# Optimization experiments

Measured on AMD Instinct MI355X. Metric: run time of the kernel, lower is better.

Reference implementation:

```python
import jax, jax.numpy as jnp
import numpy as np

B, S, H, D = 16, 2048, 768, 128
ATTR_MAX, ITEMS_MAX = 8, 32  # static equivalents of attr_type_ids.max() / item_position_ids max (data generated to hit these)


def setup_inputs() -> dict:
    key = jax.random.key(0)
    k1, k2, k3, k4 = jax.random.split(key, 4)
    return {
        "attention_mask": jnp.ones((B, S), dtype=jnp.int32),
        "hidden_states": jax.random.normal(k1, (B, S, H), dtype=jnp.float32),
        "attr_type_ids": jax.random.randint(k2, (B, S), 0, ATTR_MAX + 1),
        "item_position_ids": jax.random.randint(k3, (B, S), 0, ITEMS_MAX + 1),
        "W": jax.random.normal(k4, (H, D), dtype=jnp.float32) * (1.0 / np.sqrt(H)),
        "b": jnp.zeros((D,), dtype=jnp.float32),
    }


def reference(attention_mask, hidden_states, attr_type_ids, item_position_ids, W, b):
    # linear projection: [B,S,H] @ [H,D] -> [B,S,D]
    h = jnp.einsum('bsh,hd->bsd', hidden_states, W) + b
    Bn, Sn, Dn = h.shape

    # segmented mean over (attr_id, item_id) groups; attr/item id 0 (and >max, e.g. the 50 pad sentinel) are invalid
    valid = (attr_type_ids >= 1) & (attr_type_ids <= ATTR_MAX) & \
            (item_position_ids >= 1) & (item_position_ids <= ITEMS_MAX)
    batch_idx = jnp.arange(Bn)[:, None]
    seg = (batch_idx * ATTR_MAX + (attr_type_ids - 1)) * ITEMS_MAX + (item_position_ids - 1)
    nseg = Bn * ATTR_MAX * ITEMS_MAX
    seg = jnp.where(valid, seg, nseg)  # dump invalid tokens into extra segment
    flat_seg = seg.reshape(-1)

    sums = jax.ops.segment_sum(h.reshape(-1, Dn), flat_seg, num_segments=nseg + 1)[:nseg]
    counts = jax.ops.segment_sum(valid.reshape(-1).astype(h.dtype), flat_seg, num_segments=nseg + 1)[:nseg]

    sums = sums.reshape(Bn, ATTR_MAX, ITEMS_MAX, Dn)
    counts = counts.reshape(Bn, ATTR_MAX, ITEMS_MAX)
    empty = counts == 0
    pooled = sums / jnp.where(empty, jnp.ones_like(counts), counts)[..., None]
    return pooled, empty, h
```

## Files before the change

kernel.cpp:

```cpp
#include <hip/hip_runtime.h>
#include <hip/hip_bf16.h>

#define Bn 16
#define Sn 2048
#define Hn 768
#define Dn 128
#define AT 8
#define IT 32
#define NSEG (Bn*AT*IT)

typedef __attribute__((ext_vector_type(4))) float f32x4;
typedef __attribute__((ext_vector_type(2))) float f32x2;
typedef __attribute__((ext_vector_type(4))) int   i32x4;
typedef __attribute__((ext_vector_type(8))) short bf16x8;
typedef __attribute__((ext_vector_type(4))) short s16x4;

__device__ __forceinline__ unsigned short f2bf(float f){
  union { float f; unsigned u; } v; v.f = f;
  unsigned r = v.u + 0x7FFFu + ((v.u >> 16) & 1u);
  return (unsigned short)(r >> 16);
}

__global__ __launch_bounds__(256) void k_prep(const float* __restrict__ W,
                                              unsigned short* __restrict__ Wt){
  int gid = blockIdx.x*256 + threadIdx.x;
  if (gid >= Hn*Dn) return;
  int d = gid / Hn;
  int k = gid - d*Hn;
  Wt[gid] = f2bf(W[k*Dn + d]);
}

__global__ __launch_bounds__(256) void k_gemm(const float* __restrict__ X,
        const unsigned short* __restrict__ Wt, const float* __restrict__ bias,
        float* __restrict__ Hout){
  __shared__ unsigned char sA[2][64*128];
  __shared__ unsigned char sB[2][128*128];
  const int tid  = threadIdx.x;
  const int lane = tid & 63;
  const int wave = tid >> 6;
  const int m0 = blockIdx.x * 64;

  const int ar = tid >> 2, akq = tid & 3;
  const int bc = tid >> 1, bkh = tid & 1;
  const float*          Ap = X  + (size_t)(m0 + ar)*Hn + akq*4;
  const unsigned short* Bp = Wt + (size_t)bc*Hn + bkh*32;

  int aw[4], bw[4];
  #pragma unroll
  for (int c=0;c<4;c++) aw[c] = ar*128 + ((akq*8 + c*32) ^ ((ar&7)<<4));
  #pragma unroll
  for (int c=0;c<4;c++) bw[c] = bc*128 + ((bkh*64 + c*16) ^ ((bc&7)<<4));

  int abase[4], aswz[4];
  #pragma unroll
  for (int mi=0;mi<4;mi++){
    int row = mi*16 + (lane&15);
    abase[mi] = row*128; aswz[mi] = (row&7)<<4;
  }
  int bbase[2], bswz[2];
  #pragma unroll
  for (int ni=0;ni<2;ni++){
    int col = wave*32 + ni*16 + (lane&15);
    bbase[ni] = col*128; bswz[ni] = (col&7)<<4;
  }
  const int kblk = (lane>>4)*16;

  f32x4 acc[4][2];
  #pragma unroll
  for (int mi=0;mi<4;mi++)
    #pragma unroll
    for (int ni=0;ni<2;ni++) acc[mi][ni] = (f32x4){0.f,0.f,0.f,0.f};

  f32x4 av[4]; i32x4 bv[4];
  #pragma unroll
  for (int c=0;c<4;c++) av[c] = *(const f32x4*)(Ap + c*16);
  #pragma unroll
  for (int c=0;c<4;c++) bv[c] = *(const i32x4*)(Bp + c*8);
  #pragma unroll
  for (int c=0;c<4;c++){
    s16x4 t;
    t[0]=(short)f2bf(av[c][0]); t[1]=(short)f2bf(av[c][1]);
    t[2]=(short)f2bf(av[c][2]); t[3]=(short)f2bf(av[c][3]);
    *(s16x4*)&sA[0][aw[c]] = t;
  }
  #pragma unroll
  for (int c=0;c<4;c++) *(i32x4*)&sB[0][bw[c]] = bv[c];
  __syncthreads();

  int cur = 0;
  for (int step=0; step<12; ++step){
    if (step < 11){
      #pragma unroll
      for (int c=0;c<4;c++) av[c] = *(const f32x4*)(Ap + (step+1)*64 + c*16);
      #pragma unroll
      for (int c=0;c<4;c++) bv[c] = *(const i32x4*)(Bp + (step+1)*64 + c*8);
    }
    #pragma unroll
    for (int ks=0; ks<2; ++ks){
      bf16x8 af[4], bfv[2];
      #pragma unroll
      for (int mi=0;mi<4;mi++)
        af[mi] = *(const bf16x8*)&sA[cur][abase[mi] + ((ks*64 + kblk) ^ aswz[mi])];
      #pragma unroll
      for (int ni=0;ni<2;ni++)
        bfv[ni] = *(const bf16x8*)&sB[cur][bbase[ni] + ((ks*64 + kblk) ^ bswz[ni])];
      #pragma unroll
      for (int mi=0;mi<4;mi++)
        #pragma unroll
        for (int ni=0;ni<2;ni++)
          acc[mi][ni] = __builtin_amdgcn_mfma_f32_16x16x32_bf16(af[mi], bfv[ni], acc[mi][ni], 0, 0, 0);
    }
    if (step < 11){
      #pragma unroll
      for (int c=0;c<4;c++){
        s16x4 t;
        t[0]=(short)f2bf(av[c][0]); t[1]=(short)f2bf(av[c][1]);
        t[2]=(short)f2bf(av[c][2]); t[3]=(short)f2bf(av[c][3]);
        *(s16x4*)&sA[cur^1][aw[c]] = t;
      }
      #pragma unroll
      for (int c=0;c<4;c++) *(i32x4*)&sB[cur^1][bw[c]] = bv[c];
    }
    __syncthreads();
    cur ^= 1;
  }

  #pragma unroll
  for (int ni=0;ni<2;ni++){
    int col = wave*32 + ni*16 + (lane&15);
    float bb = bias[col];
    #pragma unroll
    for (int mi=0;mi<4;mi++){
      int row0 = m0 + mi*16 + (lane>>4)*4;
      #pragma unroll
      for (int r=0;r<4;r++)
        Hout[(size_t)(row0 + r)*Dn + col] = acc[mi][ni][r] + bb;
    }
  }
}

__global__ __launch_bounds__(256) void k_scan(const int* __restrict__ attr,
        const int* __restrict__ item, const float* __restrict__ Hsrc,
        float* __restrict__ pooled, float* __restrict__ empty){
  __shared__ float ssum[4][IT][Dn];
  __shared__ int   slist[4][512];
  __shared__ int   scnt[IT];

  const int wg  = blockIdx.x;
  const int a   = wg & 7;
  const int b   = wg >> 3;
  const int tid = threadIdx.x;
  const int wv  = tid >> 6;
  const int lane = tid & 63;

  for (int i = tid; i < 4*IT*Dn; i += 256) (&ssum[0][0][0])[i] = 0.f;
  if (tid < IT) scnt[tid] = 0;
  __syncthreads();

  const int tok0 = wv * 512;
  const int gbase = b * Sn;
  int nm = 0;
  #pragma unroll
  for (int g = 0; g < 8; ++g){
    int tok = tok0 + g*64 + lane;
    int avv = attr[gbase + tok], ivv = item[gbase + tok];
    bool m = (avv == a+1) && (ivv >= 1) && (ivv <= IT);
    unsigned long long mask = __ballot(m);
    int pos = nm + __popcll(mask & ((1ull << lane) - 1ull));
    if (m){
      slist[wv][pos] = ((ivv-1) << 16) | tok;
      atomicAdd(&scnt[ivv-1], 1);
    }
    nm += __popcll(mask);
  }

  const f32x2* hb = (const f32x2*)(Hsrc + (size_t)b*Sn*Dn);
  float* myacc = &ssum[wv][0][0];
  int e = 0;
  for (; e + 8 <= nm; e += 8){
    int idx[8]; f32x2 v[8];
    #pragma unroll
    for (int j=0;j<8;j++) idx[j] = slist[wv][e+j];
    #pragma unroll
    for (int j=0;j<8;j++) v[j] = hb[(size_t)(idx[j] & 0xffff)*64 + lane];
    #pragma unroll
    for (int j=0;j<8;j++){
      f32x2* p = (f32x2*)&myacc[(idx[j]>>16)*Dn + lane*2];
      f32x2 old = *p; old[0] += v[j][0]; old[1] += v[j][1]; *p = old;
    }
  }
  for (; e < nm; ++e){
    int idx = slist[wv][e];
    f32x2 v = hb[(size_t)(idx & 0xffff)*64 + lane];
    f32x2* p = (f32x2*)&myacc[(idx>>16)*Dn + lane*2];
    f32x2 old = *p; old[0] += v[0]; old[1] += v[1]; *p = old;
  }
  __syncthreads();

  float* outp = pooled + (size_t)wg*IT*Dn;
  for (int o = tid; o < IT*Dn; o += 256){
    int i = o >> 7, d = o & 127;
    float s = ssum[0][i][d] + ssum[1][i][d] + ssum[2][i][d] + ssum[3][i][d];
    int cnt = scnt[i];
    outp[o] = s / (float)(cnt > 0 ? cnt : 1);
  }
  if (tid < IT) empty[wg*IT + tid] = (scnt[tid] == 0) ? 1.f : 0.f;
}

extern "C" void kernel_launch(void* const* d_in, const int* in_sizes, int n_in,
                              void* d_out, int out_size, void* d_ws, size_t ws_size,
                              hipStream_t stream) {
  const float* hidden = (const float*)d_in[1];
  const int*   attr   = (const int*)  d_in[2];
  const int*   item   = (const int*)  d_in[3];
  const float* W      = (const float*)d_in[4];
  const float* bias   = (const float*)d_in[5];

  float* pooled = (float*)d_out;
  float* empty  = pooled + (size_t)NSEG*Dn;
  float* Hout   = empty  + NSEG;

  unsigned short* Wt = (unsigned short*)d_ws;

  k_prep<<<(Hn*Dn + 255)/256, 256, 0, stream>>>(W, Wt);
  k_gemm<<<(Bn*Sn)/64, 256, 0, stream>>>(hidden, Wt, bias, Hout);
  k_scan<<<Bn*AT, 256, 0, stream>>>(attr, item, Hout, pooled, empty);
}
```

Baseline: 42.27 us.

## Tile W transpose through shared memory and split segment scan across D halves

The weight prep kernel now transposes W in 64x64 tiles through padded shared memory, so global reads and writes are coalesced and the bf16 stores are vectorised. The scan kernel splits each (batch, attr) block into two blocks that each own half of the D dimension. This doubles the grid to 256 workgroups and halves the shared-memory accumulator. Count atomics move after the list build, spread across lanes. The cost is that each half-block re-reads the attr/item ids, and gathers become scalar float loads instead of float2.

```diff
diff --git a/kernel.cpp b/kernel.cpp
--- a/kernel.cpp
+++ b/kernel.cpp
@@ -10,7 +10,6 @@
 #define NSEG (Bn*AT*IT)
 
 typedef __attribute__((ext_vector_type(4))) float f32x4;
-typedef __attribute__((ext_vector_type(2))) float f32x2;
 typedef __attribute__((ext_vector_type(4))) int   i32x4;
 typedef __attribute__((ext_vector_type(8))) short bf16x8;
 typedef __attribute__((ext_vector_type(4))) short s16x4;
@@ -23,11 +22,29 @@
 
 __global__ __launch_bounds__(256) void k_prep(const float* __restrict__ W,
                                               unsigned short* __restrict__ Wt){
-  int gid = blockIdx.x*256 + threadIdx.x;
-  if (gid >= Hn*Dn) return;
-  int d = gid / Hn;
-  int k = gid - d*Hn;
-  Wt[gid] = f2bf(W[k*Dn + d]);
+  __shared__ float sT[64][65];
+  const int tid = threadIdx.x;
+  const int k0 = (blockIdx.x % 12) * 64;
+  const int d0 = (blockIdx.x / 12) * 64;
+  const int rr = tid >> 4;
+  const int cg = tid & 15;
+
+  #pragma unroll
+  for (int p = 0; p < 4; ++p){
+    int k = rr + p*16;
+    f32x4 v = *(const f32x4*)&W[(size_t)(k0 + k)*Dn + d0 + cg*4];
+    sT[k][cg*4+0] = v[0]; sT[k][cg*4+1] = v[1];
+    sT[k][cg*4+2] = v[2]; sT[k][cg*4+3] = v[3];
+  }
+  __syncthreads();
+  #pragma unroll
+  for (int p = 0; p < 4; ++p){
+    int d = rr + p*16;
+    s16x4 t;
+    #pragma unroll
+    for (int j = 0; j < 4; ++j) t[j] = (short)f2bf(sT[cg*4+j][d]);
+    *(s16x4*)&Wt[(size_t)(d0 + d)*Hn + k0 + cg*4] = t;
+  }
 }
 
 __global__ __launch_bounds__(256) void k_gemm(const float* __restrict__ X,
@@ -142,20 +159,21 @@
 __global__ __launch_bounds__(256) void k_scan(const int* __restrict__ attr,
         const int* __restrict__ item, const float* __restrict__ Hsrc,
         float* __restrict__ pooled, float* __restrict__ empty){
-  __shared__ float ssum[4][IT][Dn];
+  __shared__ float ssum[4][IT][64];
   __shared__ int   slist[4][512];
   __shared__ int   scnt[IT];
 
   const int wg  = blockIdx.x;
-  const int a   = wg & 7;
-  const int b   = wg >> 3;
+  const int dh  = wg & 1;
+  const int a   = (wg >> 1) & 7;
+  const int b   = wg >> 4;
   const int tid = threadIdx.x;
   const int wv  = tid >> 6;
   const int lane = tid & 63;
 
-  for (int i = tid; i < 4*IT*Dn; i += 256) (&ssum[0][0][0])[i] = 0.f;
+  #pragma unroll
+  for (int i = 0; i < IT; ++i) ssum[wv][i][lane] = 0.f;
   if (tid < IT) scnt[tid] = 0;
-  __syncthreads();
 
   const int tok0 = wv * 512;
   const int gbase = b * Sn;
@@ -167,44 +185,39 @@
     bool m = (avv == a+1) && (ivv >= 1) && (ivv <= IT);
     unsigned long long mask = __ballot(m);
     int pos = nm + __popcll(mask & ((1ull << lane) - 1ull));
-    if (m){
-      slist[wv][pos] = ((ivv-1) << 16) | tok;
-      atomicAdd(&scnt[ivv-1], 1);
-    }
+    if (m) slist[wv][pos] = ((ivv-1) << 16) | tok;
     nm += __popcll(mask);
   }
-
-  const f32x2* hb = (const f32x2*)(Hsrc + (size_t)b*Sn*Dn);
-  float* myacc = &ssum[wv][0][0];
+  __syncthreads();
+
+  for (int e = lane; e < nm; e += 64) atomicAdd(&scnt[slist[wv][e] >> 16], 1);
+
+  const float* hb = Hsrc + (size_t)b*Sn*Dn + dh*64 + lane;
   int e = 0;
   for (; e + 8 <= nm; e += 8){
-    int idx[8]; f32x2 v[8];
+    int idx[8]; float v[8];
     #pragma unroll
     for (int j=0;j<8;j++) idx[j] = slist[wv][e+j];
     #pragma unroll
-    for (int j=0;j<8;j++) v[j] = hb[(size_t)(idx[j] & 0xffff)*64 + lane];
-    #pragma unroll
-    for (int j=0;j<8;j++){
-      f32x2* p = (f32x2*)&myacc[(idx[j]>>16)*Dn + lane*2];
-      f32x2 old = *p; old[0] += v[j][0]; old[1] += v[j][1]; *p = old;
-    }
+    for (int j=0;j<8;j++) v[j] = hb[(size_t)(idx[j] & 0xffff)*Dn];
+    #pragma unroll
+    for (int j=0;j<8;j++) ssum[wv][idx[j]>>16][lane] += v[j];
   }
   for (; e < nm; ++e){
     int idx = slist[wv][e];
-    f32x2 v = hb[(size_t)(idx & 0xffff)*64 + lane];
-    f32x2* p = (f32x2*)&myacc[(idx>>16)*Dn + lane*2];
-    f32x2 old = *p; old[0] += v[0]; old[1] += v[1]; *p = old;
-  }
-  __syncthreads();
-
-  float* outp = pooled + (size_t)wg*IT*Dn;
-  for (int o = tid; o < IT*Dn; o += 256){
-    int i = o >> 7, d = o & 127;
+    ssum[wv][idx>>16][lane] += hb[(size_t)(idx & 0xffff)*Dn];
+  }
+  __syncthreads();
+
+  float* outp = pooled + (size_t)(b*AT + a)*IT*Dn + dh*64;
+  for (int o = tid; o < IT*64; o += 256){
+    int i = o >> 6, d = o & 63;
     float s = ssum[0][i][d] + ssum[1][i][d] + ssum[2][i][d] + ssum[3][i][d];
     int cnt = scnt[i];
-    outp[o] = s / (float)(cnt > 0 ? cnt : 1);
-  }
-  if (tid < IT) empty[wg*IT + tid] = (scnt[tid] == 0) ? 1.f : 0.f;
+    outp[i*Dn + d] = s / (float)(cnt > 0 ? cnt : 1);
+  }
+  if (dh == 0 && tid < IT)
+    empty[(b*AT + a)*IT + tid] = (scnt[tid] == 0) ? 1.f : 0.f;
 }
 
 extern "C" void kernel_launch(void* const* d_in, const int* in_sizes, int n_in,
@@ -222,7 +235,7 @@
 
   unsigned short* Wt = (unsigned short*)d_ws;
 
-  k_prep<<<(Hn*Dn + 255)/256, 256, 0, stream>>>(W, Wt);
+  k_prep<<<24, 256, 0, stream>>>(W, Wt);
   k_gemm<<<(Bn*Sn)/64, 256, 0, stream>>>(hidden, Wt, bias, Hout);
-  k_scan<<<Bn*AT, 256, 0, stream>>>(attr, item, Hout, pooled, empty);
-}
+  k_scan<<<Bn*AT*2, 256, 0, stream>>>(attr, item, Hout, pooled, empty);
+}
```

Measured after the change: 39.43 us. 1.07x faster.
